# Optimization experiments

Hardware: AMD Instinct MI355X
Metric: run time of the kernel (lower is better)

Reference implementation:

```python
import jax, jax.numpy as jnp
import numpy as np

REST = 0.0
DECAY = 0.5
THRESHOLD = 0.5
SG_WIDTH = 1.0  # rectangular surrogate-gradient window width

@jax.custom_vjp
def spike(v):
    return (v > THRESHOLD).astype(v.dtype)

def _spike_fwd(v):
    return spike(v), v

def _spike_bwd(v, g):
    # rectangular surrogate: d spike / d v = 1/width * 1[|v - threshold| < width/2]
    grad = (jnp.abs(v - THRESHOLD) < (SG_WIDTH * 0.5)).astype(g.dtype) / SG_WIDTH
    return (g * grad,)

spike.defvjp(_spike_fwd, _spike_bwd)

def setup_inputs() -> dict:
    key = jax.random.key(0)
    k1, k2, k3 = jax.random.split(key, 3)
    T, B, N = 128, 128, 1024
    tx = jax.random.normal(k1, (T, B, N), dtype=jnp.float32)
    lim = 1.0 / np.sqrt(N)  # nn.Linear default init range
    W = jax.random.uniform(k2, (N, N), dtype=jnp.float32, minval=-lim, maxval=lim)
    b = jax.random.uniform(k3, (N,), dtype=jnp.float32, minval=-lim, maxval=lim)
    return {"tx": tx, "W": W, "b": b}

def reference(tx, W, b):
    # tx: [T, B, N]; W: [N, N] (nn.Linear weight, applied as y @ W.T + b)
    v0 = jnp.full_like(tx[0], REST)
    y0 = jnp.zeros_like(tx[0])

    def step(carry, x):
        v, y = carry
        x = x + y @ W.T + b                      # recurrent input
        v = DECAY * v * (1.0 - y) + REST * y + x  # leaky integrate with reset
        y = spike(v)                              # threshold fire
        return (v, y), y

    _, ty = jax.lax.scan(step, (v0, y0), tx)
    return ty  # [T, B, N]
```

## Files before the change

### kernel.cpp

```cpp
#include <hip/hip_runtime.h>
#include <stdint.h>

#define TT 128
#define BB 128
#define NN 1024


typedef unsigned short ushort8 __attribute__((ext_vector_type(8)));

__device__ __forceinline__ float bfbits2f(uint32_t lo16) {
  union { uint32_t i; float f; } c;
  c.i = lo16 << 16;
  return c.f;
}

__device__ __forceinline__ void gload_lds16(const void* g, void* l) {
  __builtin_amdgcn_global_load_lds(
      (const __attribute__((address_space(1))) uint32_t*)g,
      (__attribute__((address_space(3))) uint32_t*)l, 16, 0, 0);
}

__global__ __launch_bounds__(256) void w_transpose_repack(
    float* __restrict__ W, uint16_t* __restrict__ WtBf,
    uint32_t* __restrict__ dirty) {
  __shared__ float ta[32][33];
  __shared__ float tb[32][33];

  int rem = blockIdx.x;
  int I = 0;
  while (rem >= (32 - I)) { rem -= (32 - I); ++I; }
  const int J = I + rem;

  const int lx = threadIdx.x & 31;
  const int ly = threadIdx.x >> 5;
  uint32_t bad = 0;

  if (I == J) {
#pragma unroll
    for (int i = 0; i < 4; ++i)
      ta[ly + i * 8][lx] = W[(I * 32 + ly + i * 8) * NN + J * 32 + lx];
    __syncthreads();
#pragma unroll
    for (int i = 0; i < 4; ++i) {
      const int idx = (I * 32 + ly + i * 8) * NN + J * 32 + lx;
      const float v = ta[lx][ly + i * 8];
      const uint32_t bits = __float_as_uint(v);
      W[idx] = v;
      WtBf[idx] = (uint16_t)(bits >> 16);
      bad |= (bits & 0xFFFFu);
    }
  } else {
#pragma unroll
    for (int i = 0; i < 4; ++i) {
      ta[ly + i * 8][lx] = W[(I * 32 + ly + i * 8) * NN + J * 32 + lx];
      tb[ly + i * 8][lx] = W[(J * 32 + ly + i * 8) * NN + I * 32 + lx];
    }
    __syncthreads();
#pragma unroll
    for (int i = 0; i < 4; ++i) {
      const int idxA = (J * 32 + ly + i * 8) * NN + I * 32 + lx;
      const float va = ta[lx][ly + i * 8];
      const uint32_t bitsA = __float_as_uint(va);
      W[idxA] = va;
      WtBf[idxA] = (uint16_t)(bitsA >> 16);
      bad |= (bitsA & 0xFFFFu);

      const int idxB = (I * 32 + ly + i * 8) * NN + J * 32 + lx;
      const float vb = tb[lx][ly + i * 8];
      const uint32_t bitsB = __float_as_uint(vb);
      W[idxB] = vb;
      WtBf[idxB] = (uint16_t)(bitsB >> 16);
      bad |= (bitsB & 0xFFFFu);
    }
  }
  const unsigned long long bm = __ballot(bad != 0);
  if ((threadIdx.x & 63) == 0 && bm) atomicOr(dirty, 1u);
}

__global__ __launch_bounds__(512) void lif_half(
    const void* __restrict__ tx_raw, const float* __restrict__ bias,
    const float* __restrict__ WtF32, const uint16_t* __restrict__ WtBf,
    const uint32_t* __restrict__ dirty,
    unsigned long long* __restrict__ gmask, float* __restrict__ out) {
  const int bb = blockIdx.x;
  const int b = bb & 127;
  const int h = bb >> 7;
  const int pp = bb ^ 128;
  const int tid = threadIdx.x;
  const int lane = tid & 63;
  const int wv = tid >> 6;
  const int n = (h << 9) + tid;

  __shared__ uint16_t wbuf[8][2][512] __attribute__((aligned(16)));
  __shared__ uint16_t lst[NN] __attribute__((aligned(16)));
  __shared__ unsigned long long smask[16];
  __shared__ int sprobe;

  if (tid == 0) sprobe = 0;
  __syncthreads();
  {
    const uint32_t* txw = (const uint32_t*)tx_raw;
    int local = 0;
#pragma unroll
    for (int i = 0; i < 2; ++i) {
      const uint32_t f = (txw[tid * 2 + i] >> 7) & 0xFFu;
      local += (f >= 0x74u && f < 0x81u) ? 1 : 0;
    }
    atomicAdd(&sprobe, local);
  }
  __syncthreads();
  const bool tx_is_bf16 = (sprobe > 512);
  const bool w_bf = (*dirty == 0u);

  const uint16_t* __restrict__ txh = (const uint16_t*)tx_raw;
  const float* __restrict__ txf = (const float*)tx_raw;
  const float bz = bias[n];

  const char* __restrict__ wbase = (const char*)WtBf;
  const float* __restrict__ rowF = WtF32 + n;
  const size_t lbyte = (size_t)(h << 10) + (size_t)(wv << 7) +
                       (size_t)((lane & 7) << 4);
  const int lrow = lane >> 3;

  float v = 0.0f;
  int y = 0;

  auto gF = [&](int s, int e) -> float {
    float acc = 0.0f;
    int i = s;
    for (; i + 8 <= e; i += 8) {
      float w[8];
#pragma unroll
      for (int u = 0; u < 8; ++u) {
        const int k = __builtin_amdgcn_readfirstlane((int)lst[i + u]);
        w[u] = rowF[k << 10];
      }
#pragma unroll
      for (int u = 0; u < 8; ++u) acc += w[u];
    }
    for (; i < e; ++i) {
      const int k = __builtin_amdgcn_readfirstlane((int)lst[i]);
      acc += rowF[k << 10];
    }
    return acc;
  };

  for (int t = 0; t < TT; ++t) {
    const int sl = t & 3;
    const unsigned long long m = __ballot(y);
    if (lane == 0) smask[h * 8 + wv] = m;
    if (lane < 2) {
      const uint32_t word = (lane == 0) ? (uint32_t)m : (uint32_t)(m >> 32);
      const unsigned long long cell =
          ((unsigned long long)(t + 1) << 32) | (unsigned long long)word;
      __hip_atomic_store(&gmask[((size_t)bb * 4 + sl) * 16 + wv * 2 + lane],
                         cell, __ATOMIC_RELAXED, __HIP_MEMORY_SCOPE_AGENT);
    }

    const int off = (t * BB + b) * NN + n;
    float xx;
    if (tx_is_bf16)
      xx = bfbits2f((uint32_t)__builtin_nontemporal_load(&txh[off]));
    else
      xx = __builtin_nontemporal_load(&txf[off]);

    __syncthreads();
    if (tid < 16) {
      const size_t ci = ((size_t)pp * 4 + sl) * 16 + tid;
      unsigned long long cell;
      while (((cell = __hip_atomic_load(&gmask[ci], __ATOMIC_RELAXED,
                                        __HIP_MEMORY_SCOPE_AGENT)) >>
              32) != (unsigned long long)(t + 1)) {
        __builtin_amdgcn_s_sleep(1);
      }
      ((uint32_t*)smask)[(1 - h) * 16 + tid] = (uint32_t)cell;
    }
    __syncthreads();

    unsigned long long mk[16];
    int cnt[16];
#pragma unroll
    for (int i = 0; i < 16; ++i) {
      mk[i] = smask[i];
      cnt[i] = __popcll(mk[i]);
    }
    int pref[16];
    {
      int s = 0;
#pragma unroll
      for (int j = 0; j < 6; ++j) { pref[j] = s; s += cnt[j]; }
    }
    {
      int s = 384;
#pragma unroll
      for (int j = 6; j < 12; ++j) { pref[j] = s; s += cnt[j]; }
    }
    {
      int s = 768;
#pragma unroll
      for (int j = 12; j < 16; ++j) { pref[j] = s; s += cnt[j]; }
    }
    const int c0 = pref[5] + cnt[5];
    const int c1 = pref[11] + cnt[11] - 384;
    const int c2 = pref[15] + cnt[15] - 768;

#pragma unroll
    for (int jj = 0; jj < 2; ++jj) {
      const int j = wv * 2 + jj;
      const unsigned long long bits = mk[j];
      if ((bits >> lane) & 1ull) {
        const int below = __builtin_amdgcn_mbcnt_hi(
            (uint32_t)(bits >> 32),
            __builtin_amdgcn_mbcnt_lo((uint32_t)bits, 0));
        lst[pref[j] + below] = (uint16_t)(j * 64 + lane);
      }
    }
    if (tid < 24) {
      const int p = tid >> 3, jn = tid & 7;
      const int c = (p == 0) ? c0 : ((p == 1) ? c1 : c2);
      if (c + jn < ((c + 7) & ~7)) lst[p * 384 + c + jn] = (uint16_t)NN;
    }
    __syncthreads();

    float P0 = 0.0f, P1 = 0.0f, P2 = 0.0f;
    if (w_bf) {
      const int n0c = (c0 + 7) >> 3;
      const int n1c = (c1 + 7) >> 3;
      const int n2c = (c2 + 7) >> 3;
      const int nct = n0c + n1c + n2c;

      uint16_t* const wb0 = &wbuf[wv][0][0];
      uint16_t* const wb1 = &wbuf[wv][1][0];

      auto pbase = [&](int c) -> int {
        if (c < n0c) return c * 8;
        if (c < n0c + n1c) return 384 + (c - n0c) * 8;
        return 768 + (c - n0c - n1c) * 8;
      };
      auto stage = [&](int c, uint16_t* dst) {
        const int k = (int)lst[pbase(c) + lrow];
        gload_lds16(wbase + ((size_t)k << 11) + lbyte, dst);
      };

      if (nct > 0) {
        stage(0, wb0);
        if (nct > 1) stage(1, wb1);
        for (int c = 0; c < nct; ++c) {
          uint16_t* const buf = (c & 1) ? wb1 : wb0;
          if (c + 1 < nct)
            asm volatile("s_waitcnt vmcnt(1)" ::: "memory");
          else
            asm volatile("s_waitcnt vmcnt(0)" ::: "memory");
          uint16_t vals[8];
#pragma unroll
          for (int r = 0; r < 8; ++r) vals[r] = buf[r * 64 + lane];
          asm volatile("s_waitcnt lgkmcnt(0)" ::: "memory");
          if (c + 2 < nct) stage(c + 2, buf);
          if (c < n0c) {
#pragma unroll
            for (int r = 0; r < 8; ++r) P0 += bfbits2f((uint32_t)vals[r]);
          } else if (c < n0c + n1c) {
#pragma unroll
            for (int r = 0; r < 8; ++r) P1 += bfbits2f((uint32_t)vals[r]);
          } else {
#pragma unroll
            for (int r = 0; r < 8; ++r) P2 += bfbits2f((uint32_t)vals[r]);
          }
        }
      }
    } else {
      P0 = gF(0, c0);
      P1 = gF(384, 384 + c1);
      P2 = gF(768, 768 + c2);
    }
    const float a = (P0 + P1) + P2;

    const float xv = (xx + a) + bz;
    v = (y ? 0.0f : 0.5f * v) + xv;
    y = (v > 0.5f);

    __builtin_nontemporal_store(y ? 1.0f : 0.0f, &out[off]);
  }
}

__global__ __launch_bounds__(1024) void lif_persample(
    const void* __restrict__ tx_raw, const float* __restrict__ bias,
    const float* __restrict__ WtF32, const uint16_t* __restrict__ WtBf,
    const uint32_t* __restrict__ dirty, float* __restrict__ out) {
  const int b = blockIdx.x;
  const int tid = threadIdx.x;
  const int lane = tid & 63;
  const int wv = tid >> 6;

  __shared__ uint16_t lst[NN] __attribute__((aligned(16)));
  __shared__ int wcnt[16];
  __shared__ int sprobe;

  if (tid == 0) sprobe = 0;
  __syncthreads();
  {
    const uint32_t* txw = (const uint32_t*)tx_raw;
    int local = 0;
#pragma unroll
    for (int i = 0; i < 2; ++i) {
      const uint32_t f = (txw[tid * 2 + i] >> 7) & 0xFFu;
      local += (f >= 0x74u && f < 0x81u) ? 1 : 0;
    }
    atomicAdd(&sprobe, local);
  }
  __syncthreads();
  const bool tx_is_bf16 = (sprobe > 1024);
  const bool w_bf = (*dirty == 0u);

  const uint16_t* __restrict__ txh = (const uint16_t*)tx_raw;
  const float* __restrict__ txf = (const float*)tx_raw;
  const float bz = bias[tid];

  const int pidx = (wv < 6) ? 0 : ((wv < 12) ? 1 : 2);
  const int pw0 = (pidx == 0) ? 0 : ((pidx == 1) ? 6 : 12);

  const uint16_t* __restrict__ rowB = WtBf + tid;
  const float* __restrict__ rowF = WtF32 + tid;

  float v = 0.0f;
  int y = 0;

  auto gB = [&](int pbase, int cnt) -> float {
    float acc = 0.0f;
    for (int i = 0; i < cnt; i += 32) {
      const ushort8* lp = (const ushort8*)(lst + pbase + i);
      const ushort8 a0 = lp[0];
      const ushort8 a1 = lp[1];
      const ushort8 a2 = lp[2];
      const ushort8 a3 = lp[3];
      float wbuf[32];
#pragma unroll
      for (int u = 0; u < 8; ++u) {
        const int k = __builtin_amdgcn_readfirstlane((int)a0[u]);
        wbuf[u] = bfbits2f((uint32_t)rowB[k << 10]);
      }
#pragma unroll
      for (int u = 0; u < 8; ++u) {
        const int k = __builtin_amdgcn_readfirstlane((int)a1[u]);
        wbuf[8 + u] = bfbits2f((uint32_t)rowB[k << 10]);
      }
#pragma unroll
      for (int u = 0; u < 8; ++u) {
        const int k = __builtin_amdgcn_readfirstlane((int)a2[u]);
        wbuf[16 + u] = bfbits2f((uint32_t)rowB[k << 10]);
      }
#pragma unroll
      for (int u = 0; u < 8; ++u) {
        const int k = __builtin_amdgcn_readfirstlane((int)a3[u]);
        wbuf[24 + u] = bfbits2f((uint32_t)rowB[k << 10]);
      }
#pragma unroll
      for (int u = 0; u < 32; ++u) acc += wbuf[u];
    }
    return acc;
  };

  auto gF = [&](int s, int e) -> float {
    float acc = 0.0f;
    int i = s;
    for (; i + 8 <= e; i += 8) {
      float w[8];
#pragma unroll
      for (int u = 0; u < 8; ++u) {
        const int k = __builtin_amdgcn_readfirstlane((int)lst[i + u]);
        w[u] = rowF[k << 10];
      }
#pragma unroll
      for (int u = 0; u < 8; ++u) acc += w[u];
    }
    for (; i < e; ++i) {
      const int k = __builtin_amdgcn_readfirstlane((int)lst[i]);
      acc += rowF[k << 10];
    }
    return acc;
  };

  for (int t = 0; t < TT; ++t) {
    const unsigned long long m = __ballot(y);
    if (lane == 0) wcnt[wv] = __popcll(m);
    __syncthreads();
    int base = 0, c0 = 0, c1 = 0, c2 = 0;
#pragma unroll
    for (int w = 0; w < 16; ++w) {
      const int c = wcnt[w];
      c0 += (w < 6) ? c : 0;
      c1 += (w >= 6 && w < 12) ? c : 0;
      c2 += (w >= 12) ? c : 0;
      base += (w >= pw0 && w < wv) ? c : 0;
    }
    if (y) {
      const int below = __builtin_amdgcn_mbcnt_hi(
          (uint32_t)(m >> 32), __builtin_amdgcn_mbcnt_lo((uint32_t)m, 0));
      lst[pidx * 384 + base + below] = (uint16_t)tid;
    }
    if (tid < 96) {
      const int p = tid >> 5, jn = tid & 31;
      const int c = (p == 0) ? c0 : ((p == 1) ? c1 : c2);
      if (c + jn < ((c + 31) & ~31)) lst[p * 384 + c + jn] = (uint16_t)NN;
    }
    __syncthreads();

    float P0, P1, P2;
    if (w_bf) {
      P0 = gB(0, (c0 + 31) & ~31);
      P1 = gB(384, (c1 + 31) & ~31);
      P2 = gB(768, (c2 + 31) & ~31);
    } else {
      P0 = gF(0, c0);
      P1 = gF(384, 384 + c1);
      P2 = gF(768, 768 + c2);
    }
    const float a = (P0 + P1) + P2;

    const int off = (t * BB + b) * NN + tid;
    const float xx = tx_is_bf16
        ? bfbits2f((uint32_t)__builtin_nontemporal_load(&txh[off]))
        : __builtin_nontemporal_load(&txf[off]);
    const float xv = (xx + a) + bz;
    v = (y ? 0.0f : 0.5f * v) + xv;
    y = (v > 0.5f);

    __builtin_nontemporal_store(y ? 1.0f : 0.0f, &out[off]);
  }
}

extern "C" void kernel_launch(void* const* d_in, const int* in_sizes, int n_in,
                              void* d_out, int out_size, void* d_ws, size_t ws_size,
                              hipStream_t stream) {
  const void* tx = nullptr;
  float* W = nullptr;
  const float* bs = nullptr;
  for (int i = 0; i < n_in; ++i) {
    if (in_sizes[i] == TT * BB * NN) tx = d_in[i];
    else if (in_sizes[i] == NN * NN) W = (float*)d_in[i];
    else if (in_sizes[i] == NN) bs = (const float*)d_in[i];
  }
  float* out = (float*)d_out;

  const size_t MB2 = 2u * 1024u * 1024u;
  uint16_t* WtBf = (uint16_t*)d_ws;
  uint16_t* zrow = WtBf + NN * NN;
  uint32_t* dirty = (uint32_t*)((char*)d_ws + MB2 + 2048u);
  unsigned long long* gmask =
      (unsigned long long*)((char*)d_ws + MB2 + 4096u);
  const size_t GMASK_BYTES = 256u * 4u * 16u * 8u;
  const size_t need = MB2 + 4096u + GMASK_BYTES;

  hipMemsetAsync(dirty, 0, sizeof(uint32_t), stream);
  hipMemsetAsync(zrow, 0, NN * sizeof(uint16_t), stream);

  w_transpose_repack<<<dim3(528), dim3(256), 0, stream>>>(W, WtBf, dirty);

  if (ws_size >= need) {
    hipMemsetAsync(gmask, 0, GMASK_BYTES, stream);
    lif_half<<<dim3(256), dim3(512), 0, stream>>>(tx, bs, W, WtBf, dirty,
                                                  gmask, out);
  } else {
    lif_persample<<<dim3(BB), dim3(1024), 0, stream>>>(tx, bs, W, WtBf, dirty,
                                                       out);
  }
}
```

Before: 1.750 ms.

## Group eight samples per block sharing union of spiking rows of W

Replaces the two-blocks-per-sample split over neurons with a layout where each block handles 8 batch samples and a 64-neuron column slice; the 16 blocks per sample group exchange spike masks through global memory. Each block builds the union of spiking input neurons across its 8 samples, stages those W rows once into LDS in a triple-buffered pipeline, and every sample's wave accumulates only its own spikes from the shared tiles. The aim is to reuse each fetched W row across several samples and cut global weight traffic. In exchange, each block now waits on 15 peers per step instead of one, and the per-lane accumulation loop becomes more complex and branchy.

```diff
diff --git a/kernel.cpp b/kernel.cpp
--- a/kernel.cpp
+++ b/kernel.cpp
@@ -77,23 +77,25 @@
   if ((threadIdx.x & 63) == 0 && bm) atomicOr(dirty, 1u);
 }
 
-__global__ __launch_bounds__(512) void lif_half(
+__global__ __launch_bounds__(512) void lif_group(
     const void* __restrict__ tx_raw, const float* __restrict__ bias,
     const float* __restrict__ WtF32, const uint16_t* __restrict__ WtBf,
     const uint32_t* __restrict__ dirty,
     unsigned long long* __restrict__ gmask, float* __restrict__ out) {
   const int bb = blockIdx.x;
-  const int b = bb & 127;
-  const int h = bb >> 7;
-  const int pp = bb ^ 128;
+  const int g = bb & 15;
+  const int r = bb >> 4;
   const int tid = threadIdx.x;
   const int lane = tid & 63;
-  const int wv = tid >> 6;
-  const int n = (h << 9) + tid;
-
-  __shared__ uint16_t wbuf[8][2][512] __attribute__((aligned(16)));
-  __shared__ uint16_t lst[NN] __attribute__((aligned(16)));
-  __shared__ unsigned long long smask[16];
+  const int sl = tid >> 6;
+  const int b = g * 8 + sl;
+  const int n = (r << 6) + lane;
+
+  __shared__ uint16_t sbuf[3][64][64] __attribute__((aligned(16)));
+  __shared__ uint16_t ulst[1024] __attribute__((aligned(16)));
+  __shared__ uint16_t lst_s[8][1040] __attribute__((aligned(16)));
+  __shared__ unsigned long long m8[8][16];
+  __shared__ unsigned long long uch[16];
   __shared__ int sprobe;
 
   if (tid == 0) sprobe = 0;
@@ -115,45 +117,20 @@
   const uint16_t* __restrict__ txh = (const uint16_t*)tx_raw;
   const float* __restrict__ txf = (const float*)tx_raw;
   const float bz = bias[n];
-
   const char* __restrict__ wbase = (const char*)WtBf;
-  const float* __restrict__ rowF = WtF32 + n;
-  const size_t lbyte = (size_t)(h << 10) + (size_t)(wv << 7) +
-                       (size_t)((lane & 7) << 4);
-  const int lrow = lane >> 3;
 
   float v = 0.0f;
   int y = 0;
 
-  auto gF = [&](int s, int e) -> float {
-    float acc = 0.0f;
-    int i = s;
-    for (; i + 8 <= e; i += 8) {
-      float w[8];
-#pragma unroll
-      for (int u = 0; u < 8; ++u) {
-        const int k = __builtin_amdgcn_readfirstlane((int)lst[i + u]);
-        w[u] = rowF[k << 10];
-      }
-#pragma unroll
-      for (int u = 0; u < 8; ++u) acc += w[u];
-    }
-    for (; i < e; ++i) {
-      const int k = __builtin_amdgcn_readfirstlane((int)lst[i]);
-      acc += rowF[k << 10];
-    }
-    return acc;
-  };
-
   for (int t = 0; t < TT; ++t) {
-    const int sl = t & 3;
+    const int slq = t & 3;
     const unsigned long long m = __ballot(y);
-    if (lane == 0) smask[h * 8 + wv] = m;
+    if (lane == 0) m8[sl][r] = m;
     if (lane < 2) {
-      const uint32_t word = (lane == 0) ? (uint32_t)m : (uint32_t)(m >> 32);
+      const uint32_t word = lane ? (uint32_t)(m >> 32) : (uint32_t)m;
       const unsigned long long cell =
           ((unsigned long long)(t + 1) << 32) | (unsigned long long)word;
-      __hip_atomic_store(&gmask[((size_t)bb * 4 + sl) * 16 + wv * 2 + lane],
+      __hip_atomic_store(&gmask[((size_t)bb * 4 + slq) * 16 + sl * 2 + lane],
                          cell, __ATOMIC_RELAXED, __HIP_MEMORY_SCOPE_AGENT);
     }
 
@@ -165,113 +142,131 @@
       xx = __builtin_nontemporal_load(&txf[off]);
 
     __syncthreads();
-    if (tid < 16) {
-      const size_t ci = ((size_t)pp * 4 + sl) * 16 + tid;
+    if (tid < 240) {
+      const int rr0 = tid >> 4;
+      const int cw = tid & 15;
+      const int rr = rr0 + (rr0 >= r ? 1 : 0);
+      const int pb = (rr << 4) + g;
+      const size_t ci = ((size_t)pb * 4 + slq) * 16 + cw;
       unsigned long long cell;
       while (((cell = __hip_atomic_load(&gmask[ci], __ATOMIC_RELAXED,
                                         __HIP_MEMORY_SCOPE_AGENT)) >>
               32) != (unsigned long long)(t + 1)) {
         __builtin_amdgcn_s_sleep(1);
       }
-      ((uint32_t*)smask)[(1 - h) * 16 + tid] = (uint32_t)cell;
-    }
-    __syncthreads();
-
-    unsigned long long mk[16];
-    int cnt[16];
-#pragma unroll
-    for (int i = 0; i < 16; ++i) {
-      mk[i] = smask[i];
-      cnt[i] = __popcll(mk[i]);
-    }
-    int pref[16];
+      ((uint32_t*)&m8[cw >> 1][rr])[cw & 1] = (uint32_t)cell;
+    }
+    __syncthreads();
+    if (tid < 16) {
+      unsigned long long u = 0;
+#pragma unroll
+      for (int s = 0; s < 8; ++s) u |= m8[s][tid];
+      uch[tid] = u;
+    }
+    __syncthreads();
+
+    int U = 0;
     {
-      int s = 0;
-#pragma unroll
-      for (int j = 0; j < 6; ++j) { pref[j] = s; s += cnt[j]; }
-    }
+      int up = 0;
+#pragma unroll
+      for (int j = 0; j < 16; ++j) {
+        const unsigned long long ub = uch[j];
+        if ((j >> 1) == sl) {
+          if ((ub >> lane) & 1ull) {
+            const int below = __popcll(ub & ((1ull << lane) - 1ull));
+            ulst[up + below] = (uint16_t)(j * 64 + lane);
+          }
+        }
+        up += __popcll(ub);
+      }
+      U = up;
+    }
+    const int nch = (U + 63) >> 6;
+    if (tid < nch * 64 - U) ulst[U + tid] = (uint16_t)NN;
+
+    int ct = 0, c0s = 0, c01s = 0;
     {
-      int s = 384;
-#pragma unroll
-      for (int j = 6; j < 12; ++j) { pref[j] = s; s += cnt[j]; }
+      const unsigned long long lm = (1ull << lane) - 1ull;
+      int up = 0;
+#pragma unroll
+      for (int j = 0; j < 16; ++j) {
+        const unsigned long long bits = m8[sl][j];
+        const unsigned long long ub = uch[j];
+        if ((bits >> lane) & 1ull) {
+          const int rank = ct + __popcll(bits & lm);
+          lst_s[sl][rank] = (uint16_t)(up + __popcll(ub & lm));
+        }
+        ct += __popcll(bits);
+        up += __popcll(ub);
+        if (j == 5) c0s = ct;
+        if (j == 11) c01s = ct;
+      }
     }
     {
-      int s = 768;
-#pragma unroll
-      for (int j = 12; j < 16; ++j) { pref[j] = s; s += cnt[j]; }
-    }
-    const int c0 = pref[5] + cnt[5];
-    const int c1 = pref[11] + cnt[11] - 384;
-    const int c2 = pref[15] + cnt[15] - 768;
-
-#pragma unroll
-    for (int jj = 0; jj < 2; ++jj) {
-      const int j = wv * 2 + jj;
-      const unsigned long long bits = mk[j];
-      if ((bits >> lane) & 1ull) {
-        const int below = __builtin_amdgcn_mbcnt_hi(
-            (uint32_t)(bits >> 32),
-            __builtin_amdgcn_mbcnt_lo((uint32_t)bits, 0));
-        lst[pref[j] + below] = (uint16_t)(j * 64 + lane);
-      }
-    }
-    if (tid < 24) {
-      const int p = tid >> 3, jn = tid & 7;
-      const int c = (p == 0) ? c0 : ((p == 1) ? c1 : c2);
-      if (c + jn < ((c + 7) & ~7)) lst[p * 384 + c + jn] = (uint16_t)NN;
+      const int pad = (-ct) & 7;
+      if (lane < pad) lst_s[sl][ct + lane] = 0xFFFFu;
     }
     __syncthreads();
 
     float P0 = 0.0f, P1 = 0.0f, P2 = 0.0f;
     if (w_bf) {
-      const int n0c = (c0 + 7) >> 3;
-      const int n1c = (c1 + 7) >> 3;
-      const int n2c = (c2 + 7) >> 3;
-      const int nct = n0c + n1c + n2c;
-
-      uint16_t* const wb0 = &wbuf[wv][0][0];
-      uint16_t* const wb1 = &wbuf[wv][1][0];
-
-      auto pbase = [&](int c) -> int {
-        if (c < n0c) return c * 8;
-        if (c < n0c + n1c) return 384 + (c - n0c) * 8;
-        return 768 + (c - n0c - n1c) * 8;
+      const size_t gsub = ((size_t)r << 7) + (size_t)((lane & 7) << 4);
+      const int lrow = lane >> 3;
+      auto stagec = [&](int ch) {
+        const int kk = (int)ulst[ch * 64 + sl * 8 + lrow];
+        const int cb = ch - (ch / 3) * 3;
+        gload_lds16(wbase + ((size_t)kk << 11) + gsub, &sbuf[cb][sl * 8][0]);
       };
-      auto stage = [&](int c, uint16_t* dst) {
-        const int k = (int)lst[pbase(c) + lrow];
-        gload_lds16(wbase + ((size_t)k << 11) + lbyte, dst);
-      };
-
-      if (nct > 0) {
-        stage(0, wb0);
-        if (nct > 1) stage(1, wb1);
-        for (int c = 0; c < nct; ++c) {
-          uint16_t* const buf = (c & 1) ? wb1 : wb0;
-          if (c + 1 < nct)
-            asm volatile("s_waitcnt vmcnt(1)" ::: "memory");
-          else
-            asm volatile("s_waitcnt vmcnt(0)" ::: "memory");
-          uint16_t vals[8];
-#pragma unroll
-          for (int r = 0; r < 8; ++r) vals[r] = buf[r * 64 + lane];
-          asm volatile("s_waitcnt lgkmcnt(0)" ::: "memory");
-          if (c + 2 < nct) stage(c + 2, buf);
-          if (c < n0c) {
-#pragma unroll
-            for (int r = 0; r < 8; ++r) P0 += bfbits2f((uint32_t)vals[r]);
-          } else if (c < n0c + n1c) {
-#pragma unroll
-            for (int r = 0; r < 8; ++r) P1 += bfbits2f((uint32_t)vals[r]);
-          } else {
-#pragma unroll
-            for (int r = 0; r < 8; ++r) P2 += bfbits2f((uint32_t)vals[r]);
+      if (nch > 0) stagec(0);
+      if (nch > 1) stagec(1);
+
+      int basei = 0;
+      bool have = false;
+      uint32_t p0 = 0, p1 = 0, p2 = 0, p3 = 0, p4 = 0, p5 = 0, p6 = 0, p7 = 0;
+      for (int ch = 0; ch < nch; ++ch) {
+        if (ch + 1 < nch)
+          asm volatile("s_waitcnt vmcnt(1)\n\ts_barrier" ::: "memory");
+        else
+          asm volatile("s_waitcnt vmcnt(0)\n\ts_barrier" ::: "memory");
+        if (ch + 2 < nch) stagec(ch + 2);
+
+        const int chend = (ch + 1) * 64;
+        for (;;) {
+          if (!have) {
+            if (basei >= ct) break;
+            const ushort8 pw = *(const ushort8*)(&lst_s[sl][basei]);
+            p0 = pw[0]; p1 = pw[1]; p2 = pw[2]; p3 = pw[3];
+            p4 = pw[4]; p5 = pw[5]; p6 = pw[6]; p7 = pw[7];
+            have = true;
           }
+#define STEPU(u, pu)                                                        \
+          if ((int)pu < chend) {                                            \
+            const int bsel = (int)pu >> 6;                                  \
+            const uint16_t wv_ =                                            \
+                sbuf[bsel - (bsel / 3) * 3][(int)pu & 63][lane];            \
+            const float f_ = bfbits2f((uint32_t)wv_);                       \
+            const int ix = basei + u;                                       \
+            if (ix < c0s) P0 += f_;                                         \
+            else if (ix < c01s) P1 += f_;                                   \
+            else P2 += f_;                                                  \
+            pu = 0xFFFFu;                                                   \
+          }
+          STEPU(0, p0) STEPU(1, p1) STEPU(2, p2) STEPU(3, p3)
+          STEPU(4, p4) STEPU(5, p5) STEPU(6, p6) STEPU(7, p7)
+#undef STEPU
+          if (p7 == 0xFFFFu) { basei += 8; have = false; }
+          else break;
         }
       }
     } else {
-      P0 = gF(0, c0);
-      P1 = gF(384, 384 + c1);
-      P2 = gF(768, 768 + c2);
+      for (int i2 = 0; i2 < ct; ++i2) {
+        const int pos = (int)lst_s[sl][i2];
+        const int kk = (int)ulst[pos];
+        const float w = WtF32[(size_t)kk * NN + n];
+        if (i2 < c0s) P0 += w;
+        else if (i2 < c01s) P1 += w;
+        else P2 += w;
+      }
     }
     const float a = (P0 + P1) + P2;
 
@@ -458,8 +453,8 @@
 
   if (ws_size >= need) {
     hipMemsetAsync(gmask, 0, GMASK_BYTES, stream);
-    lif_half<<<dim3(256), dim3(512), 0, stream>>>(tx, bs, W, WtBf, dirty,
-                                                  gmask, out);
+    lif_group<<<dim3(256), dim3(512), 0, stream>>>(tx, bs, W, WtBf, dirty,
+                                                   gmask, out);
   } else {
     lif_persample<<<dim3(BB), dim3(1024), 0, stream>>>(tx, bs, W, WtBf, dirty,
                                                        out);
```

Result: slower. 6.269 ms (+258.1%).
